# Performance work log

Hardware: AMD Instinct MI355X
Metric: run time of the kernel (lower is better)

The kernel has to match this reference:

```python
import jax, jax.numpy as jnp
import numpy as np


def setup_inputs() -> dict:
    key = jax.random.key(0)
    ks = jax.random.split(key, 7)
    B, D, d1, d2, d3 = 256, 256, 1024, 512, 256
    s = lambda f: 1.0 / np.sqrt(f)  # torch nn.Linear-style init scale
    return {
        "x": jax.random.normal(ks[0], (B, D), jnp.float32),
        "W1": jax.random.normal(ks[1], (d1, D), jnp.float32) * s(D),
        "b1": jax.random.normal(ks[2], (d1,), jnp.float32) * s(D),
        "W2": jax.random.normal(ks[3], (d2, d1), jnp.float32) * s(d1),
        "b2": jax.random.normal(ks[4], (d2,), jnp.float32) * s(d1),
        "W3": jax.random.normal(ks[5], (d3, d2), jnp.float32) * s(d2),
        "b3": jax.random.normal(ks[6], (d3,), jnp.float32) * s(d2),
        "k": 10,
    }


def _border_dists(x, W1, b1, W2, b2, W3, b3):
    # Layer 1: pre-activations and boundary distances. For the first layer the
    # effective linear map is W1 itself (shared across the batch).
    z1 = x @ W1.T + b1                                   # [B, d1]
    dist1 = jnp.abs(z1) / jnp.linalg.norm(W1, axis=1)    # [B, d1]
    m1 = (z1 > 0).astype(x.dtype)
    V1 = m1[:, :, None] * W1[None]                       # [B, d1, D] per-instance map after ReLU
    h1 = m1 * z1

    # Layer 2
    z2 = h1 @ W2.T + b2                                  # [B, d2]
    V2 = jnp.einsum('oi,bid->bod', W2, V1)               # [B, d2, D]
    dist2 = jnp.abs(z2) / jnp.linalg.norm(V2, axis=2)
    m2 = (z2 > 0).astype(x.dtype)
    h2 = m2 * z2

    # Layer 3
    z3 = h2 @ W3.T + b3                                  # [B, d3]
    V3 = jnp.einsum('oi,bid->bod', W3, m2[:, :, None] * V2)  # [B, d3, D]
    dist3 = jnp.abs(z3) / jnp.linalg.norm(V3, axis=2)

    return jnp.concatenate([dist1, dist2, dist3], axis=1)  # [B, d1+d2+d3]


def reference(x, W1, b1, W2, b2, W3, b3, k):
    dists = _border_dists(x, W1, b1, W2, b2, W3, b3)
    # smallest-k distances per instance via top_k on negated distances
    neg_top, _ = jax.lax.top_k(-dists, k)                # [B, k]
    return jnp.sum(-neg_top)                             # border-distance loss (scalar)
```

## Files before the change

kernel.cpp:

```cpp
#include <hip/hip_runtime.h>
#include <math.h>
#include <float.h>

#define B   256
#define D   256
#define D1  1024
#define D2  512
#define D3  256
#define NDIST (D1 + D2 + D3)
#define CQ  2.0f

typedef __attribute__((ext_vector_type(8))) short short8;
typedef __attribute__((ext_vector_type(4))) float f32x4;
typedef __attribute__((ext_vector_type(4))) int   i32x4;

__device__ __forceinline__ float waveReduceSum(float v) {
    #pragma unroll
    for (int off = 32; off > 0; off >>= 1)
        v += __shfl_down(v, off, 64);
    return v;
}
__device__ __forceinline__ float waveReduceMax(float v) {
    #pragma unroll
    for (int off = 32; off > 0; off >>= 1)
        v = fmaxf(v, __shfl_down(v, off, 64));
    return v;
}
__device__ __forceinline__ unsigned short f2bf(float f) {
    unsigned int u = __float_as_uint(f);
    u = (u + 0x7FFFu + ((u >> 16) & 1u)) >> 16;
    return (unsigned short)u;
}
__device__ __forceinline__ float bf2f(unsigned short h) {
    return __uint_as_float(((unsigned int)h) << 16);
}
__device__ __forceinline__ void gld16(const void* g, void* l) {
    __builtin_amdgcn_global_load_lds(
        (const __attribute__((address_space(1))) unsigned int*)g,
        (__attribute__((address_space(3))) unsigned int*)l, 16, 0, 0);
}
__device__ __forceinline__ int swz_src(int row, int lane) {
    return ((lane & 3) + ((row >> 1) & 3)) & 3;
}
__device__ __forceinline__ int swz_frag(int row, int quad) {
    return row * 32 + (((quad - ((row >> 1) & 3)) & 3) * 8);
}

__device__ __forceinline__ void split_job(const float* src, unsigned short* hi,
                                          unsigned short* lo, int off) {
    float4 v = *(const float4*)(src + off);
    ushort4 h, l;
    h.x = f2bf(v.x); l.x = f2bf(v.x - bf2f(h.x));
    h.y = f2bf(v.y); l.y = f2bf(v.y - bf2f(h.y));
    h.z = f2bf(v.z); l.z = f2bf(v.z - bf2f(h.z));
    h.w = f2bf(v.w); l.w = f2bf(v.w - bf2f(h.w));
    *(ushort4*)(hi + off) = h;
    *(ushort4*)(lo + off) = l;
}

__device__ __forceinline__ void split8(const float* p, short8& h8, short8& l8) {
    float4 a = *(const float4*)(p);
    float4 b = *(const float4*)(p + 4);
    float hv[8] = { a.x, a.y, a.z, a.w, b.x, b.y, b.z, b.w };
    #pragma unroll
    for (int q = 0; q < 8; q++) {
        unsigned short hh = f2bf(hv[q]);
        h8[q] = (short)hh;
        l8[q] = (short)f2bf(hv[q] - bf2f(hh));
    }
}

template <int KD, int KL>
__device__ __forceinline__ void mfma3_64(
    const unsigned short* __restrict__ Ahi, const unsigned short* __restrict__ Alo,
    const unsigned short* __restrict__ Bhi, const unsigned short* __restrict__ Blo,
    int m0, int n0, int k0, unsigned short* sm, f32x4 acc[2][2]) {
    int tid = threadIdx.x;
    int l = tid & 63, w = tid >> 6;
    int rsub = l >> 2;
    int quad = l >> 4, l16 = l & 15;
    int wm = (w >> 1) * 32, wn = (w & 1) * 32;
    unsigned short* sAh = sm;
    unsigned short* sAl = sm + 2048;
    unsigned short* sBh = sm + 4096;
    unsigned short* sBl = sm + 6144;
    ptrdiff_t dA = Alo - Ahi, dB = Blo - Bhi;
    int rloc = w * 16 + rsub;
    int c = swz_src(rloc, l);
    const unsigned short* pa = Ahi + (size_t)(m0 + rloc) * KD + k0 + c * 8;
    const unsigned short* pb = Bhi + (size_t)(n0 + rloc) * KD + k0 + c * 8;
    int aoff[2], boff[2];
    #pragma unroll
    for (int mt = 0; mt < 2; mt++) aoff[mt] = swz_frag(wm + mt * 16 + l16, quad);
    #pragma unroll
    for (int nt = 0; nt < 2; nt++) boff[nt] = swz_frag(wn + nt * 16 + l16, quad);
    for (int kk = 0; kk < KL; kk += 32) {
        gld16(pa + kk,      sAh + w * 512);
        gld16(pa + dA + kk, sAl + w * 512);
        gld16(pb + kk,      sBh + w * 512);
        gld16(pb + dB + kk, sBl + w * 512);
        __syncthreads();
        short8 ah[2], al[2], bh[2], bl[2];
        #pragma unroll
        for (int mt = 0; mt < 2; mt++) {
            ah[mt] = *(const short8*)(sAh + aoff[mt]);
            al[mt] = *(const short8*)(sAl + aoff[mt]);
        }
        #pragma unroll
        for (int nt = 0; nt < 2; nt++) {
            bh[nt] = *(const short8*)(sBh + boff[nt]);
            bl[nt] = *(const short8*)(sBl + boff[nt]);
        }
        #pragma unroll
        for (int mt = 0; mt < 2; mt++)
            #pragma unroll
            for (int nt = 0; nt < 2; nt++) {
                acc[mt][nt] = __builtin_amdgcn_mfma_f32_16x16x32_bf16(ah[mt], bh[nt], acc[mt][nt], 0, 0, 0);
                acc[mt][nt] = __builtin_amdgcn_mfma_f32_16x16x32_bf16(ah[mt], bl[nt], acc[mt][nt], 0, 0, 0);
                acc[mt][nt] = __builtin_amdgcn_mfma_f32_16x16x32_bf16(al[mt], bh[nt], acc[mt][nt], 0, 0, 0);
            }
        __syncthreads();
    }
}

__global__ __launch_bounds__(256) void k_l1p(
    const float* __restrict__ x, const float* __restrict__ W1,
    const float* __restrict__ W2, const float* __restrict__ W3,
    const float* __restrict__ b1,
    float* __restrict__ dists, unsigned char* __restrict__ m1q,
    unsigned short* __restrict__ h1hi, unsigned short* __restrict__ h1lo,
    float* __restrict__ zeros, float* __restrict__ outp,
    unsigned short* __restrict__ W2hi, unsigned short* __restrict__ W2lo,
    unsigned short* __restrict__ W3hi, unsigned short* __restrict__ W3lo,
    signed char* __restrict__ W1Ti8, float* __restrict__ saq,
    signed char* __restrict__ W2i8,  float* __restrict__ sbq,
    signed char* __restrict__ W3i8,  float* __restrict__ s3q,
    float* __restrict__ rn1) {
    __shared__ __align__(16) unsigned short sm[8192];
    int blk = blockIdx.x;
    int t = threadIdx.x;

    if (blk < 64) {
        unsigned short* sAh = sm;
        unsigned short* sAl = sm + 2048;
        unsigned short* sBh = sm + 4096;
        unsigned short* sBl = sm + 6144;
        int m0 = (blk & 3) * 64, n0 = (blk >> 2) * 64;
        int l = t & 63, w = t >> 6;
        int rsub = l >> 2;
        int quad = l >> 4, l16 = l & 15;
        int wm = (w >> 1) * 32, wn = (w & 1) * 32;
        int rloc = w * 16 + rsub;
        int c = swz_src(rloc, l);
        const float* pax = x + (size_t)(m0 + rloc) * D + c * 8;
        const float* pbw = W1 + (size_t)(n0 + rloc) * D + c * 8;
        int aoff[2], boff[2];
        #pragma unroll
        for (int mt = 0; mt < 2; mt++) aoff[mt] = swz_frag(wm + mt * 16 + l16, quad);
        #pragma unroll
        for (int nt = 0; nt < 2; nt++) boff[nt] = swz_frag(wn + nt * 16 + l16, quad);
        int wrA = w * 512 + l * 8;
        f32x4 acc[2][2] = {};
        for (int kk = 0; kk < D; kk += 32) {
            short8 ha, la, hb, lb;
            split8(pax + kk, ha, la);
            split8(pbw + kk, hb, lb);
            *(short8*)(sAh + wrA) = ha;
            *(short8*)(sAl + wrA) = la;
            *(short8*)(sBh + wrA) = hb;
            *(short8*)(sBl + wrA) = lb;
            __syncthreads();
            short8 ah[2], al[2], bh[2], bl[2];
            #pragma unroll
            for (int mt = 0; mt < 2; mt++) {
                ah[mt] = *(const short8*)(sAh + aoff[mt]);
                al[mt] = *(const short8*)(sAl + aoff[mt]);
            }
            #pragma unroll
            for (int nt = 0; nt < 2; nt++) {
                bh[nt] = *(const short8*)(sBh + boff[nt]);
                bl[nt] = *(const short8*)(sBl + boff[nt]);
            }
            #pragma unroll
            for (int mt = 0; mt < 2; mt++)
                #pragma unroll
                for (int nt = 0; nt < 2; nt++) {
                    acc[mt][nt] = __builtin_amdgcn_mfma_f32_16x16x32_bf16(ah[mt], bh[nt], acc[mt][nt], 0, 0, 0);
                    acc[mt][nt] = __builtin_amdgcn_mfma_f32_16x16x32_bf16(ah[mt], bl[nt], acc[mt][nt], 0, 0, 0);
                    acc[mt][nt] = __builtin_amdgcn_mfma_f32_16x16x32_bf16(al[mt], bh[nt], acc[mt][nt], 0, 0, 0);
                }
            __syncthreads();
        }
        #pragma unroll
        for (int mt = 0; mt < 2; mt++)
            #pragma unroll
            for (int nt = 0; nt < 2; nt++) {
                int n = n0 + wn + nt * 16 + l16;
                float bv = b1[n];
                #pragma unroll
                for (int r = 0; r < 4; r++) {
                    int m = m0 + wm + mt * 16 + quad * 4 + r;
                    float z = acc[mt][nt][r] + bv;
                    size_t idx = (size_t)m * D1 + n;
                    dists[idx] = fabsf(z);
                    m1q[idx] = (z > 0.f) ? 0xFFu : 0u;
                    float h = z > 0.f ? z : 0.f;
                    unsigned short hh = f2bf(h);
                    h1hi[idx] = hh;
                    h1lo[idx] = f2bf(h - bf2f(hh));
                }
            }
        return;
    }
    if (blk < 448) {
        if (blk == 64 && t == 0) outp[0] = 0.f;
        int i4 = (blk - 64) * 1024 + t * 4;
        *(float4*)(zeros + i4) = make_float4(0.f, 0.f, 0.f, 0.f);
        return;
    }
    if (blk < 960) {
        split_job(W2, W2hi, W2lo, (blk - 448) * 1024 + t * 4);
        return;
    }
    if (blk < 1088) {
        split_job(W3, W3hi, W3lo, (blk - 960) * 1024 + t * 4);
        return;
    }
    if (blk < 1120) {
        int ty = t >> 5, tx = t & 31;
        int d = (blk - 1088) * 8 + ty;
        float m = 0.f;
        for (int i = tx; i < D1; i += 32) m = fmaxf(m, fabsf(W1[(size_t)i * D + d]));
        #pragma unroll
        for (int off = 16; off > 0; off >>= 1) m = fmaxf(m, __shfl_down(m, off, 32));
        m = __shfl(m, 0, 32);
        m = fmaxf(m, 1e-20f);
        if (tx == 0) saq[d] = m / 127.f;
        float inv = 127.f / m;
        for (int i = tx; i < D1; i += 32) {
            int q = __float2int_rn(W1[(size_t)i * D + d] * inv);
            W1Ti8[(size_t)d * D1 + i] = (signed char)q;
        }
        return;
    }
    if (blk < 1248) {
        int o = (blk - 1120) * 4 + (t >> 6);
        int l = t & 63;
        const float* row = W2 + (size_t)o * D1;
        float m = 0.f;
        for (int tt = l; tt < D1; tt += 64) m = fmaxf(m, fabsf(row[tt]));
        m = waveReduceMax(m);
        m = __shfl(m, 0, 64);
        m = fmaxf(m, 1e-20f);
        if (l == 0) sbq[o] = m / 127.f;
        float inv = 127.f / m;
        for (int tt = l; tt < D1; tt += 64)
            W2i8[(size_t)o * D1 + tt] = (signed char)__float2int_rn(row[tt] * inv);
        return;
    }
    if (blk < 1312) {
        int p = (blk - 1248) * 4 + (t >> 6);
        int l = t & 63;
        const float* row = W3 + (size_t)p * D2;
        float m = 0.f;
        for (int tt = l; tt < D2; tt += 64) m = fmaxf(m, fabsf(row[tt]));
        m = waveReduceMax(m);
        m = __shfl(m, 0, 64);
        m = fmaxf(m, 1e-20f);
        if (l == 0) s3q[p] = m / 127.f;
        float inv = 127.f / m;
        for (int tt = l; tt < D2; tt += 64)
            W3i8[(size_t)p * D2 + tt] = (signed char)__float2int_rn(row[tt] * inv);
        return;
    }
    {
        int gw = (blk - 1312) * 4 + (t >> 6);
        int lane = t & 63;
        const float* row = W1 + (size_t)gw * D;
        float s = 0.f;
        for (int tt = lane; tt < D; tt += 64) { float v = row[tt]; s += v * v; }
        s = waveReduceSum(s);
        if (lane == 0) rn1[gw] = sqrtf(s);
    }
}

__global__ __launch_bounds__(256) void k_big1(
    const unsigned short* __restrict__ h1hi, const unsigned short* __restrict__ h1lo,
    const unsigned short* __restrict__ W2hi, const unsigned short* __restrict__ W2lo,
    float* __restrict__ z2,
    const signed char* __restrict__ W1Ti8,
    const signed char* __restrict__ W2i8,
    const unsigned char* __restrict__ m1q,
    const float* __restrict__ saq,
    const float* __restrict__ sbq,
    signed char* __restrict__ qV2,
    float* __restrict__ norm2) {
    __shared__ __align__(16) unsigned char smem[32768];
    int bid = blockIdx.x;

    if (bid < 128) {
        unsigned short* sm = (unsigned short*)smem;
        int m0 = (bid & 3) * 64, n0 = ((bid >> 2) & 7) * 64, k0 = (bid >> 5) * 256;
        f32x4 acc[2][2] = {};
        mfma3_64<D1, 256>(h1hi, h1lo, W2hi, W2lo, m0, n0, k0, sm, acc);
        int l = threadIdx.x & 63, w = threadIdx.x >> 6;
        int quad = l >> 4, l16 = l & 15;
        int wm = (w >> 1) * 32, wn = (w & 1) * 32;
        #pragma unroll
        for (int mt = 0; mt < 2; mt++)
            #pragma unroll
            for (int nt = 0; nt < 2; nt++) {
                int n = n0 + wn + nt * 16 + l16;
                #pragma unroll
                for (int r = 0; r < 4; r++) {
                    int m = m0 + wm + mt * 16 + quad * 4 + r;
                    atomicAdd(&z2[(size_t)m * D2 + n], acc[mt][nt][r]);
                }
            }
        return;
    }

    int j = bid - 128;
    signed char* As = (signed char*)smem;
    signed char* Bs = (signed char*)smem + 16384;
    int m0 = (j & 1) * 128;
    int o0 = ((j >> 1) & 3) * 128;
    int b = j >> 3;
    int tid = threadIdx.x;
    int l = tid & 63, w = tid >> 6;
    int quad = l >> 4, l16 = l & 15;
    int wm = (w >> 1) * 64, wn = (w & 1) * 64;
    const unsigned char* mrow = m1q + (size_t)b * D1;

    const signed char* pa[4];
    const signed char* pb[4];
    int lrow = l >> 3, ls = l & 7;
    #pragma unroll
    for (int r = 0; r < 4; r++) {
        int row = r * 32 + w * 8 + lrow;
        int c = (ls + (row & 7)) & 7;
        pa[r] = W1Ti8 + (size_t)(m0 + row) * D1 + c * 16;
        pb[r] = W2i8 + (size_t)(o0 + row) * D1 + c * 16;
    }
    int aoff[4][2], boff[4][2];
    #pragma unroll
    for (int mt = 0; mt < 4; mt++) {
        int tr = wm + mt * 16 + l16;
        #pragma unroll
        for (int ks = 0; ks < 2; ks++)
            aoff[mt][ks] = tr * 128 + (((ks * 4 + quad) - (tr & 7)) & 7) * 16;
    }
    #pragma unroll
    for (int nt = 0; nt < 4; nt++) {
        int tr = wn + nt * 16 + l16;
        #pragma unroll
        for (int ks = 0; ks < 2; ks++)
            boff[nt][ks] = tr * 128 + (((ks * 4 + quad) - (tr & 7)) & 7) * 16;
    }

    i32x4 acc[4][4];
    #pragma unroll
    for (int i = 0; i < 4; i++)
        #pragma unroll
        for (int jj = 0; jj < 4; jj++) acc[i][jj] = (i32x4)0;

    for (int kk = 0; kk < D1; kk += 128) {
        #pragma unroll
        for (int r = 0; r < 4; r++) {
            gld16(pa[r] + kk, As + r * 4096 + w * 1024);
            gld16(pb[r] + kk, Bs + r * 4096 + w * 1024);
        }
        i32x4 mv0 = *(const i32x4*)(mrow + kk + quad * 16);
        i32x4 mv1 = *(const i32x4*)(mrow + kk + 64 + quad * 16);
        __syncthreads();
        #pragma unroll
        for (int ks = 0; ks < 2; ks++) {
            i32x4 mv = ks ? mv1 : mv0;
            i32x4 a[4], bq[4];
            #pragma unroll
            for (int mt = 0; mt < 4; mt++)
                a[mt] = (*(const i32x4*)(As + aoff[mt][ks])) & mv;
            #pragma unroll
            for (int nt = 0; nt < 4; nt++)
                bq[nt] = *(const i32x4*)(Bs + boff[nt][ks]);
            #pragma unroll
            for (int mt = 0; mt < 4; mt++)
                #pragma unroll
                for (int nt = 0; nt < 4; nt++)
                    acc[mt][nt] = __builtin_amdgcn_mfma_i32_16x16x64_i8(
                        a[mt], bq[nt], acc[mt][nt], 0, 0, 0);
        }
        __syncthreads();
    }

    float sad[4][4];
    #pragma unroll
    for (int mt = 0; mt < 4; mt++)
        #pragma unroll
        for (int r = 0; r < 4; r++)
            sad[mt][r] = saq[m0 + wm + mt * 16 + quad * 4 + r];
    float sbv[4], sbdq[4];
    #pragma unroll
    for (int nt = 0; nt < 4; nt++) {
        sbv[nt] = sbq[o0 + wn + nt * 16 + l16];
        sbdq[nt] = sbv[nt] * (1.0f / CQ);
    }

    #pragma unroll
    for (int nt = 0; nt < 4; nt++) {
        float s = 0.f;
        #pragma unroll
        for (int mt = 0; mt < 4; mt++)
            #pragma unroll
            for (int r = 0; r < 4; r++) {
                float v = (float)acc[mt][nt][r] * sad[mt][r] * sbv[nt];
                s += v * v;
            }
        s += __shfl_down(s, 32, 64);
        s += __shfl_down(s, 16, 64);
        if (l < 16)
            atomicAdd(&norm2[(size_t)b * D2 + o0 + wn + nt * 16 + l], s);
    }

    signed char* qb = qV2 + (size_t)b * (D * D2);
    #pragma unroll
    for (int mt = 0; mt < 4; mt++) {
        int dbase = m0 + wm + mt * 16 + quad * 4;
        #pragma unroll
        for (int r = 0; r < 4; r++)
            #pragma unroll
            for (int nt = 0; nt < 4; nt++) {
                int o = o0 + wn + nt * 16 + l16;
                int qi = __float2int_rn((float)acc[mt][nt][r] * sbdq[nt]);
                qi = max(-127, min(127, qi));
                qb[(size_t)(dbase + r) * D2 + o] = (signed char)qi;
            }
    }
}

__global__ __launch_bounds__(256) void k_big2(
    const float* __restrict__ z2,
    const float* __restrict__ b2,
    const unsigned short* __restrict__ W3hi, const unsigned short* __restrict__ W3lo,
    float* __restrict__ z3,
    const signed char* __restrict__ W3i8,
    const signed char* __restrict__ qV2,
    const float* __restrict__ saq,
    const float* __restrict__ s3q,
    float* __restrict__ norm3) {
    __shared__ __align__(16) unsigned char smem[33280];
    int bid = blockIdx.x;
    int tid = threadIdx.x;

    if (bid < 32) {
        unsigned short* sAh = (unsigned short*)smem;
        unsigned short* sAl = sAh + 2048;
        unsigned short* sBh = sAh + 4096;
        unsigned short* sBl = sAh + 6144;
        int m0 = (bid & 3) * 64, n0 = ((bid >> 2) & 3) * 64, k0 = (bid >> 4) * 256;
        int l = tid & 63, w = tid >> 6;
        int rsub = l >> 2;
        int quad = l >> 4, l16 = l & 15;
        int wm = (w >> 1) * 32, wn = (w & 1) * 32;
        int rloc = w * 16 + rsub;
        int c = swz_src(rloc, l);
        const float* pz  = z2 + (size_t)(m0 + rloc) * D2 + k0 + c * 8;
        const float* pbi = b2 + k0 + c * 8;
        const unsigned short* pb = W3hi + (size_t)(n0 + rloc) * D2 + k0 + c * 8;
        ptrdiff_t dB = W3lo - W3hi;
        int aoff[2], boff[2];
        #pragma unroll
        for (int mt = 0; mt < 2; mt++) aoff[mt] = swz_frag(wm + mt * 16 + l16, quad);
        #pragma unroll
        for (int nt = 0; nt < 2; nt++) boff[nt] = swz_frag(wn + nt * 16 + l16, quad);
        int wrA = w * 512 + l * 8;
        f32x4 acc[2][2] = {};
        for (int kk = 0; kk < 256; kk += 32) {
            gld16(pb + kk,      sBh + w * 512);
            gld16(pb + dB + kk, sBl + w * 512);
            float4 za = *(const float4*)(pz + kk);
            float4 zb = *(const float4*)(pz + kk + 4);
            float4 ba = *(const float4*)(pbi + kk);
            float4 bb = *(const float4*)(pbi + kk + 4);
            float hv[8] = { za.x + ba.x, za.y + ba.y, za.z + ba.z, za.w + ba.w,
                            zb.x + bb.x, zb.y + bb.y, zb.z + bb.z, zb.w + bb.w };
            short8 h8, l8;
            #pragma unroll
            for (int q2 = 0; q2 < 8; q2++) {
                float h = hv[q2] > 0.f ? hv[q2] : 0.f;
                unsigned short hh = f2bf(h);
                h8[q2] = (short)hh;
                l8[q2] = (short)f2bf(h - bf2f(hh));
            }
            *(short8*)(sAh + wrA) = h8;
            *(short8*)(sAl + wrA) = l8;
            __syncthreads();
            short8 ah[2], al[2], bh[2], bl[2];
            #pragma unroll
            for (int mt = 0; mt < 2; mt++) {
                ah[mt] = *(const short8*)(sAh + aoff[mt]);
                al[mt] = *(const short8*)(sAl + aoff[mt]);
            }
            #pragma unroll
            for (int nt = 0; nt < 2; nt++) {
                bh[nt] = *(const short8*)(sBh + boff[nt]);
                bl[nt] = *(const short8*)(sBl + boff[nt]);
            }
            #pragma unroll
            for (int mt = 0; mt < 2; mt++)
                #pragma unroll
                for (int nt = 0; nt < 2; nt++) {
                    acc[mt][nt] = __builtin_amdgcn_mfma_f32_16x16x32_bf16(ah[mt], bh[nt], acc[mt][nt], 0, 0, 0);
                    acc[mt][nt] = __builtin_amdgcn_mfma_f32_16x16x32_bf16(ah[mt], bl[nt], acc[mt][nt], 0, 0, 0);
                    acc[mt][nt] = __builtin_amdgcn_mfma_f32_16x16x32_bf16(al[mt], bh[nt], acc[mt][nt], 0, 0, 0);
                }
            __syncthreads();
        }
        #pragma unroll
        for (int mt = 0; mt < 2; mt++)
            #pragma unroll
            for (int nt = 0; nt < 2; nt++) {
                int n = n0 + wn + nt * 16 + l16;
                #pragma unroll
                for (int r = 0; r < 4; r++) {
                    int m = m0 + wm + mt * 16 + quad * 4 + r;
                    atomicAdd(&z3[(size_t)m * D3 + n], acc[mt][nt][r]);
                }
            }
        return;
    }

    int j = bid - 32;
    signed char* As = (signed char*)smem;
    signed char* Bs = (signed char*)smem + 16384;
    unsigned char* mbuf = (unsigned char*)smem + 32768;
    int m0 = (j & 1) * 128;
    int n0 = ((j >> 1) & 1) * 128;
    int bc = j >> 2;
    int l = tid & 63, w = tid >> 6;
    int quad = l >> 4, l16 = l & 15;
    int wm = (w >> 1) * 64, wn = (w & 1) * 64;
    const signed char* Bsrc = qV2 + (size_t)bc * (D * D2);

    {
        #pragma unroll
        for (int rr = 0; rr < 2; rr++) {
            int o = tid * 2 + rr;
            float z = z2[(size_t)bc * D2 + o] + b2[o];
            mbuf[o] = (z > 0.f) ? 0xFFu : 0u;
        }
    }
    __syncthreads();

    const signed char* pa[4];
    const signed char* pb[4];
    int lrow = l >> 3, ls = l & 7;
    #pragma unroll
    for (int r = 0; r < 4; r++) {
        int row = r * 32 + w * 8 + lrow;
        int c = (ls + (row & 7)) & 7;
        pa[r] = W3i8 + (size_t)(m0 + row) * D2 + c * 16;
        pb[r] = Bsrc + (size_t)(n0 + row) * D2 + c * 16;
    }
    int aoff[4][2], boff[4][2];
    #pragma unroll
    for (int mt = 0; mt < 4; mt++) {
        int tr = wm + mt * 16 + l16;
        #pragma unroll
        for (int ks = 0; ks < 2; ks++)
            aoff[mt][ks] = tr * 128 + (((ks * 4 + quad) - (tr & 7)) & 7) * 16;
    }
    #pragma unroll
    for (int nt = 0; nt < 4; nt++) {
        int tr = wn + nt * 16 + l16;
        #pragma unroll
        for (int ks = 0; ks < 2; ks++)
            boff[nt][ks] = tr * 128 + (((ks * 4 + quad) - (tr & 7)) & 7) * 16;
    }

    i32x4 acc[4][4];
    #pragma unroll
    for (int i = 0; i < 4; i++)
        #pragma unroll
        for (int jj = 0; jj < 4; jj++) acc[i][jj] = (i32x4)0;

    for (int kk = 0; kk < D2; kk += 128) {
        #pragma unroll
        for (int r = 0; r < 4; r++) {
            gld16(pa[r] + kk, As + r * 4096 + w * 1024);
            gld16(pb[r] + kk, Bs + r * 4096 + w * 1024);
        }
        __syncthreads();
        i32x4 mv0 = *(const i32x4*)(mbuf + kk + quad * 16);
        i32x4 mv1 = *(const i32x4*)(mbuf + kk + 64 + quad * 16);
        #pragma unroll
        for (int ks = 0; ks < 2; ks++) {
            i32x4 mv = ks ? mv1 : mv0;
            i32x4 a[4], bq[4];
            #pragma unroll
            for (int mt = 0; mt < 4; mt++)
                a[mt] = *(const i32x4*)(As + aoff[mt][ks]);
            #pragma unroll
            for (int nt = 0; nt < 4; nt++)
                bq[nt] = (*(const i32x4*)(Bs + boff[nt][ks])) & mv;
            #pragma unroll
            for (int mt = 0; mt < 4; mt++)
                #pragma unroll
                for (int nt = 0; nt < 4; nt++)
                    acc[mt][nt] = __builtin_amdgcn_mfma_i32_16x16x64_i8(
                        a[mt], bq[nt], acc[mt][nt], 0, 0, 0);
        }
        __syncthreads();
    }

    float saCQ[4];
    #pragma unroll
    for (int nt = 0; nt < 4; nt++)
        saCQ[nt] = saq[n0 + wn + nt * 16 + l16] * CQ;

    #pragma unroll
    for (int mt = 0; mt < 4; mt++)
        #pragma unroll
        for (int r = 0; r < 4; r++) {
            float s = 0.f;
            #pragma unroll
            for (int nt = 0; nt < 4; nt++) {
                float v = (float)acc[mt][nt][r] * saCQ[nt];
                s += v * v;
            }
            s += __shfl_down(s, 8, 64);
            s += __shfl_down(s, 4, 64);
            s += __shfl_down(s, 2, 64);
            s += __shfl_down(s, 1, 64);
            if (l16 == 0) {
                int p = m0 + wm + mt * 16 + quad * 4 + r;
                float s3 = s3q[p];
                atomicAdd(&norm3[(size_t)bc * D3 + p], s * s3 * s3);
            }
        }
}

__global__ __launch_bounds__(256) void k_topk(
    const float* __restrict__ dists,
    const float* __restrict__ rn1,
    const float* __restrict__ z2, const float* __restrict__ b2,
    const float* __restrict__ norm2,
    const float* __restrict__ z3, const float* __restrict__ b3,
    const float* __restrict__ norm3,
    const int* __restrict__ kp, float* __restrict__ outp) {
    int t = threadIdx.x;
    int wv = t >> 6, lane = t & 63;
    int b = blockIdx.x * 4 + wv;
    float lv[28];
    #pragma unroll
    for (int j = 0; j < 16; j++) {
        int n = lane + 64 * j;
        lv[j] = dists[(size_t)b * D1 + n] / rn1[n];
    }
    #pragma unroll
    for (int j = 16; j < 24; j++) {
        int o = lane + 64 * (j - 16);
        float zz = z2[(size_t)b * D2 + o] + b2[o];
        lv[j] = fabsf(zz) / sqrtf(norm2[(size_t)b * D2 + o]);
    }
    #pragma unroll
    for (int j = 24; j < 28; j++) {
        int p = lane + 64 * (j - 24);
        float zz = z3[(size_t)b * D3 + p] + b3[p];
        lv[j] = fabsf(zz) / sqrtf(norm3[(size_t)b * D3 + p]);
    }
    int k = *kp;
    if (k > NDIST) k = NDIST;
    float sum = 0.f;
    for (int it = 0; it < k; it++) {
        float mv = lv[0]; int mj = 0;
        #pragma unroll
        for (int j = 1; j < 28; j++)
            if (lv[j] < mv) { mv = lv[j]; mj = j; }
        unsigned long long key =
            ((unsigned long long)__float_as_uint(mv) << 32) | (unsigned)(lane * 32 + mj);
        #pragma unroll
        for (int off = 1; off < 64; off <<= 1) {
            unsigned long long o = __shfl_xor(key, off, 64);
            if (o < key) key = o;
        }
        sum += __uint_as_float((unsigned)(key >> 32));
        int wl = (int)((key >> 5) & 63u), wj = (int)(key & 31u);
        if (lane == wl) lv[wj] = FLT_MAX;
    }
    if (lane == 0) atomicAdd(outp, sum);
}

extern "C" void kernel_launch(void* const* d_in, const int* in_sizes, int n_in,
                              void* d_out, int out_size, void* d_ws, size_t ws_size,
                              hipStream_t stream) {
    const float* x  = (const float*)d_in[0];
    const float* W1 = (const float*)d_in[1];
    const float* b1 = (const float*)d_in[2];
    const float* W2 = (const float*)d_in[3];
    const float* b2 = (const float*)d_in[4];
    const float* W3 = (const float*)d_in[5];
    const float* b3 = (const float*)d_in[6];
    const int*   kp = (const int*)d_in[7];
    float* outp = (float*)d_out;

    float* fp = (float*)d_ws;
    float* rn1     = fp;                          fp += D1;
    float* dists   = fp;                          fp += (size_t)B * D1;
    float* saq     = fp;                          fp += D;
    float* sbq     = fp;                          fp += D2;
    float* s3q     = fp;                          fp += D3;
    float* z2      = fp;                          fp += (size_t)B * D2;
    float* z3      = fp;                          fp += (size_t)B * D3;
    float* norm2   = fp;                          fp += (size_t)B * D2;
    float* norm3   = fp;                          fp += (size_t)B * D3;
    unsigned short* up = (unsigned short*)fp;
    unsigned short* W2hi  = up;  up += (size_t)D2 * D1;
    unsigned short* W2lo  = up;  up += (size_t)D2 * D1;
    unsigned short* W3hi  = up;  up += (size_t)D3 * D2;
    unsigned short* W3lo  = up;  up += (size_t)D3 * D2;
    unsigned short* h1hi  = up;  up += (size_t)B * D1;
    unsigned short* h1lo  = up;  up += (size_t)B * D1;
    signed char*    cp = (signed char*)up;
    signed char*    W1Ti8 = cp;  cp += (size_t)D * D1;
    signed char*    W2i8  = cp;  cp += (size_t)D2 * D1;
    signed char*    W3i8  = cp;  cp += (size_t)D3 * D2;
    unsigned char*  m1q   = (unsigned char*)cp;  cp += (size_t)B * D1;
    signed char*    qV2   = cp;

    k_l1p<<<1568, 256, 0, stream>>>(x, W1, W2, W3, b1,
                                    dists, m1q, h1hi, h1lo,
                                    z2, outp, W2hi, W2lo, W3hi, W3lo,
                                    W1Ti8, saq, W2i8, sbq, W3i8, s3q, rn1);

    k_big1<<<2176, 256, 0, stream>>>(h1hi, h1lo, W2hi, W2lo, z2,
                                     W1Ti8, W2i8, m1q, saq, sbq, qV2, norm2);

    k_big2<<<1056, 256, 0, stream>>>(z2, b2, W3hi, W3lo, z3,
                                     W3i8, qV2, saq, s3q, norm3);

    k_topk<<<B / 4, 256, 0, stream>>>(dists, rn1, z2, b2, norm2, z3, b3, norm3,
                                      kp, outp);
}
```

Baseline: 175.1 us.

## Double-buffer LDS tiles in int8 GEMM paths and fuse norm/quant epilogue

The int8 MFMA loops in k_big1 and k_big2 now use two LDS buffers, so the global-to-LDS loads for the next K tile are issued while MFMAs run on the current tile. The loops are fully unrolled and need one barrier per iteration instead of two. In k_big1 the squared-norm accumulation and the int8 quantize/store of V2 are merged into a single pass over the accumulators, with the sbv² factor applied once at the end. LDS per block roughly doubles to about 64 KB, which may reduce how many blocks fit on a CU.

```diff
diff --git a/kernel.cpp b/kernel.cpp
--- a/kernel.cpp
+++ b/kernel.cpp
@@ -295,7 +295,7 @@
     const float* __restrict__ sbq,
     signed char* __restrict__ qV2,
     float* __restrict__ norm2) {
-    __shared__ __align__(16) unsigned char smem[32768];
+    __shared__ __align__(16) unsigned char smem[65536];
     int bid = blockIdx.x;
 
     if (bid < 128) {
@@ -321,8 +321,6 @@
     }
 
     int j = bid - 128;
-    signed char* As = (signed char*)smem;
-    signed char* Bs = (signed char*)smem + 16384;
     int m0 = (j & 1) * 128;
     int o0 = ((j >> 1) & 3) * 128;
     int b = j >> 3;
@@ -364,15 +362,35 @@
         #pragma unroll
         for (int jj = 0; jj < 4; jj++) acc[i][jj] = (i32x4)0;
 
-    for (int kk = 0; kk < D1; kk += 128) {
+    {
+        signed char* buf0 = (signed char*)smem;
         #pragma unroll
         for (int r = 0; r < 4; r++) {
-            gld16(pa[r] + kk, As + r * 4096 + w * 1024);
-            gld16(pb[r] + kk, Bs + r * 4096 + w * 1024);
-        }
-        i32x4 mv0 = *(const i32x4*)(mrow + kk + quad * 16);
-        i32x4 mv1 = *(const i32x4*)(mrow + kk + 64 + quad * 16);
-        __syncthreads();
+            gld16(pa[r], buf0 + r * 4096 + w * 1024);
+            gld16(pb[r], buf0 + 16384 + r * 4096 + w * 1024);
+        }
+    }
+    i32x4 mv0 = *(const i32x4*)(mrow + quad * 16);
+    i32x4 mv1 = *(const i32x4*)(mrow + 64 + quad * 16);
+    __syncthreads();
+
+    #pragma unroll
+    for (int t = 0; t < 8; t++) {
+        signed char* bufc = (signed char*)smem + ((t & 1) << 15);
+        signed char* bufn = (signed char*)smem + (((t + 1) & 1) << 15);
+        i32x4 nmv0 = mv0, nmv1 = mv1;
+        if (t < 7) {
+            int kn = (t + 1) * 128;
+            #pragma unroll
+            for (int r = 0; r < 4; r++) {
+                gld16(pa[r] + kn, bufn + r * 4096 + w * 1024);
+                gld16(pb[r] + kn, bufn + 16384 + r * 4096 + w * 1024);
+            }
+            nmv0 = *(const i32x4*)(mrow + kn + quad * 16);
+            nmv1 = *(const i32x4*)(mrow + kn + 64 + quad * 16);
+        }
+        const signed char* As = bufc;
+        const signed char* Bs = bufc + 16384;
         #pragma unroll
         for (int ks = 0; ks < 2; ks++) {
             i32x4 mv = ks ? mv1 : mv0;
@@ -391,6 +409,7 @@
                         a[mt], bq[nt], acc[mt][nt], 0, 0, 0);
         }
         __syncthreads();
+        mv0 = nmv0; mv1 = nmv1;
     }
 
     float sad[4][4];
@@ -406,35 +425,33 @@
         sbdq[nt] = sbv[nt] * (1.0f / CQ);
     }
 
+    float nrm[4] = {0.f, 0.f, 0.f, 0.f};
+    signed char* qb = qV2 + (size_t)b * (D * D2);
+    #pragma unroll
+    for (int mt = 0; mt < 4; mt++) {
+        int dbase = m0 + wm + mt * 16 + quad * 4;
+        #pragma unroll
+        for (int r = 0; r < 4; r++) {
+            float sa = sad[mt][r];
+            size_t rowoff = (size_t)(dbase + r) * D2;
+            #pragma unroll
+            for (int nt = 0; nt < 4; nt++) {
+                float tv = (float)acc[mt][nt][r];
+                float u = tv * sa;
+                nrm[nt] = fmaf(u, u, nrm[nt]);
+                int qi = __float2int_rn(tv * sbdq[nt]);
+                qi = max(-127, min(127, qi));
+                qb[rowoff + o0 + wn + nt * 16 + l16] = (signed char)qi;
+            }
+        }
+    }
     #pragma unroll
     for (int nt = 0; nt < 4; nt++) {
-        float s = 0.f;
-        #pragma unroll
-        for (int mt = 0; mt < 4; mt++)
-            #pragma unroll
-            for (int r = 0; r < 4; r++) {
-                float v = (float)acc[mt][nt][r] * sad[mt][r] * sbv[nt];
-                s += v * v;
-            }
+        float s = nrm[nt] * (sbv[nt] * sbv[nt]);
         s += __shfl_down(s, 32, 64);
         s += __shfl_down(s, 16, 64);
         if (l < 16)
             atomicAdd(&norm2[(size_t)b * D2 + o0 + wn + nt * 16 + l], s);
-    }
-
-    signed char* qb = qV2 + (size_t)b * (D * D2);
-    #pragma unroll
-    for (int mt = 0; mt < 4; mt++) {
-        int dbase = m0 + wm + mt * 16 + quad * 4;
-        #pragma unroll
-        for (int r = 0; r < 4; r++)
-            #pragma unroll
-            for (int nt = 0; nt < 4; nt++) {
-                int o = o0 + wn + nt * 16 + l16;
-                int qi = __float2int_rn((float)acc[mt][nt][r] * sbdq[nt]);
-                qi = max(-127, min(127, qi));
-                qb[(size_t)(dbase + r) * D2 + o] = (signed char)qi;
-            }
     }
 }
 
@@ -448,7 +465,7 @@
     const float* __restrict__ saq,
     const float* __restrict__ s3q,
     float* __restrict__ norm3) {
-    __shared__ __align__(16) unsigned char smem[33280];
+    __shared__ __align__(16) unsigned char smem[66048];
     int bid = blockIdx.x;
     int tid = threadIdx.x;
 
@@ -531,9 +548,7 @@
     }
 
     int j = bid - 32;
-    signed char* As = (signed char*)smem;
-    signed char* Bs = (signed char*)smem + 16384;
-    unsigned char* mbuf = (unsigned char*)smem + 32768;
+    unsigned char* mbuf = (unsigned char*)smem + 65536;
     int m0 = (j & 1) * 128;
     int n0 = ((j >> 1) & 1) * 128;
     int bc = j >> 2;
@@ -550,7 +565,6 @@
             mbuf[o] = (z > 0.f) ? 0xFFu : 0u;
         }
     }
-    __syncthreads();
 
     const signed char* pa[4];
     const signed char* pb[4];
@@ -584,15 +598,33 @@
         #pragma unroll
         for (int jj = 0; jj < 4; jj++) acc[i][jj] = (i32x4)0;
 
-    for (int kk = 0; kk < D2; kk += 128) {
+    {
+        signed char* buf0 = (signed char*)smem;
         #pragma unroll
         for (int r = 0; r < 4; r++) {
-            gld16(pa[r] + kk, As + r * 4096 + w * 1024);
-            gld16(pb[r] + kk, Bs + r * 4096 + w * 1024);
-        }
-        __syncthreads();
+            gld16(pa[r], buf0 + r * 4096 + w * 1024);
+            gld16(pb[r], buf0 + 16384 + r * 4096 + w * 1024);
+        }
+    }
+    __syncthreads();
+
+    #pragma unroll
+    for (int t = 0; t < 4; t++) {
+        signed char* bufc = (signed char*)smem + ((t & 1) << 15);
+        signed char* bufn = (signed char*)smem + (((t + 1) & 1) << 15);
+        if (t < 3) {
+            int kn = (t + 1) * 128;
+            #pragma unroll
+            for (int r = 0; r < 4; r++) {
+                gld16(pa[r] + kn, bufn + r * 4096 + w * 1024);
+                gld16(pb[r] + kn, bufn + 16384 + r * 4096 + w * 1024);
+            }
+        }
+        int kk = t * 128;
         i32x4 mv0 = *(const i32x4*)(mbuf + kk + quad * 16);
         i32x4 mv1 = *(const i32x4*)(mbuf + kk + 64 + quad * 16);
+        const signed char* As = bufc;
+        const signed char* Bs = bufc + 16384;
         #pragma unroll
         for (int ks = 0; ks < 2; ks++) {
             i32x4 mv = ks ? mv1 : mv0;
```

After: 175.4 us. Within noise of the previous version (+0.2%).
